# Performance work log

Hardware: AMD Instinct MI355X
Metric: run time of the kernel (lower is better)

The kernel has to match this reference:

```python
import jax, jax.numpy as jnp
import numpy as np
from jax import lax


def _conv(x, w, b):
    y = lax.conv_general_dilated(x, w, window_strides=(1, 1), padding='SAME',
                                 dimension_numbers=('NCHW', 'OIHW', 'NCHW'))
    return y + b[None, :, None, None]


def _maxpool2(x):
    return lax.reduce_window(x, -jnp.inf, lax.max,
                             window_dimensions=(1, 1, 2, 2),
                             window_strides=(1, 1, 2, 2), padding='VALID')


def setup_inputs() -> dict:
    key = jax.random.key(0)
    ks = jax.random.split(key, 11)
    f32 = jnp.float32
    return {
        'x': jax.random.normal(ks[0], (512, 1, 112, 112), f32),
        'w_conv1': jax.random.normal(ks[1], (8, 1, 3, 3), f32) * 0.1,
        'b_conv1': jax.random.normal(ks[2], (8,), f32) * 0.1,
        'w_conv2': jax.random.normal(ks[3], (16, 8, 3, 3), f32) * 0.1,
        'b_conv2': jax.random.normal(ks[4], (16,), f32) * 0.1,
        'w_patch': jax.random.normal(ks[5], (4, 64), f32) * 0.1,
        'b_patch': jax.random.normal(ks[6], (4,), f32) * 0.1,
        'w_fc1': jax.random.normal(ks[7], (64, 784), f32) * 0.05,
        'b_fc1': jax.random.normal(ks[8], (64,), f32) * 0.05,
        'w_fc2': jax.random.normal(ks[9], (10, 64), f32) * 0.05,
        'b_fc2': jax.random.normal(ks[10], (10,), f32) * 0.05,
    }


def reference(x, w_conv1, b_conv1, w_conv2, b_conv2, w_patch, b_patch,
              w_fc1, b_fc1, w_fc2, b_fc2):
    B = x.shape[0]
    h = _maxpool2(jax.nn.relu(_conv(x, w_conv1, b_conv1)))        # [B,8,56,56]
    f = _maxpool2(jax.nn.relu(_conv(h, w_conv2, b_conv2)))        # [B,16,28,28]
    C, H, W = f.shape[1], f.shape[2], f.shape[3]
    # im2col: 2x2 non-overlapping spatial patches, flattened as (C,2,2) -> 64
    p = f.reshape(B, C, H // 2, 2, W // 2, 2)
    p = p.transpose(0, 2, 4, 1, 3, 5).reshape(B, (H // 2) * (W // 2), C * 4)  # [B,196,64]
    pf = jnp.einsum('bpk,ok->bpo', p, w_patch) + b_patch          # [B,196,4]
    pf = pf.reshape(B, -1)                                        # [B,784]
    h1 = jax.nn.relu(pf @ w_fc1.T + b_fc1)
    logits = h1 @ w_fc2.T + b_fc2
    return jax.nn.log_softmax(logits, axis=-1)
```

## Files before the change

kernel.cpp:

```cpp
#include <hip/hip_runtime.h>


#define HSTR 58
#define NROWS 30
#define FSTR 33

typedef _Float16 half2_t __attribute__((ext_vector_type(2)));
typedef _Float16 f16x8 __attribute__((ext_vector_type(8)));
typedef float f32x4 __attribute__((ext_vector_type(4)));
typedef float f32x2 __attribute__((ext_vector_type(2)));

__device__ __forceinline__ unsigned pack_f16(float a, float b) {
  union { half2_t h; unsigned u; } z;
  z.h[0] = (_Float16)a;
  z.h[1] = (_Float16)b;
  return z.u;
}

__device__ __forceinline__ half2_t as_h2(unsigned u) {
  union { unsigned u; half2_t h; } z;
  z.u = u;
  return z.h;
}

__device__ __forceinline__ f16x8 as_f16x8(uint4 u) {
  union { uint4 u; f16x8 f; } z;
  z.u = u;
  return z.f;
}

__device__ __forceinline__ float fdot2_(half2_t a, half2_t b, float c) {
#if __has_builtin(__builtin_amdgcn_fdot2)
  return __builtin_amdgcn_fdot2(a, b, c, false);
#else
  return c + (float)a[0] * (float)b[0] + (float)a[1] * (float)b[1];
#endif
}

__global__ __launch_bounds__(256, 4) void k_fused(
    const float* __restrict__ x, const float* __restrict__ w1,
    const float* __restrict__ b1, const float* __restrict__ w2,
    const float* __restrict__ b2, const float* __restrict__ wp,
    const float* __restrict__ bp, const float* __restrict__ w_fc1,
    float* __restrict__ h1p) {
  __shared__ __align__(16) unsigned hsu[4 * NROWS * HSTR];
  __shared__ __align__(16) unsigned bwl[768];
  __shared__ __align__(16) unsigned wps[128];
  __shared__ __align__(16) unsigned fsu[49 * FSTR];
  __shared__ __align__(16) float pfl[392];
  const int tid = threadIdx.x;
  const int b = blockIdx.x >> 1;
  const int s = blockIdx.x & 1;
  const int l = tid & 63;
  const int wv = __builtin_amdgcn_readfirstlane(tid >> 6);
  const float* xb = x + (long)b * 12544;
  const float bpv = bp[tid & 3];

  for (int i = tid; i < 4 * NROWS * HSTR; i += 256) hsu[i] = 0u;
  for (int t = tid; t < 768; t += 256) {
    int oc = t / 48, k32 = t % 48;
    unsigned v = 0u;
    if (k32 < 36) {
      int icp = k32 / 9, tap = k32 - icp * 9;
      v = pack_f16(w2[(oc * 8 + 2 * icp) * 9 + tap],
                   w2[(oc * 8 + 2 * icp + 1) * 9 + tap]);
    }
    bwl[t] = v;
  }
  if (tid < 128) {
    int i = tid >> 2, ot = tid & 3;
    int l0 = 2 * i, l1 = 2 * i + 1;
    wps[tid] = pack_f16(wp[ot * 64 + (l0 & 15) * 4 + (l0 >> 4)],
                        wp[ot * 64 + (l1 & 15) * 4 + (l1 >> 4)]);
  }
  __syncthreads();

  for (int task = tid; task < 1680; task += 256) {
    int r = task / 56, hc = task % 56;
    int gr = 28 * s - 1 + r;
    if ((unsigned)gr >= 56u) continue;
    float win[4][4];
    int iy0 = 2 * gr - 1, ix0 = 2 * hc - 1;
#pragma unroll
    for (int rr = 0; rr < 4; ++rr) {
      int iy = iy0 + rr;
      bool yok = (unsigned)iy < 112u;
#pragma unroll
      for (int qq = 0; qq < 4; ++qq) {
        int ix = ix0 + qq;
        win[rr][qq] = (yok && (unsigned)ix < 112u) ? xb[iy * 112 + ix] : 0.f;
      }
    }
    float hv[8];
#pragma unroll
    for (int c = 0; c < 8; ++c) {
      f32x2 sA = {0.f, 0.f};
      f32x2 sB = {0.f, 0.f};
#pragma unroll
      for (int ty = 0; ty < 3; ++ty)
#pragma unroll
        for (int tx = 0; tx < 3; ++tx) {
          float wk = w1[c * 9 + ty * 3 + tx];
          f32x2 wkk = {wk, wk};
          f32x2 xa = {win[ty][tx], win[ty][tx + 1]};
          f32x2 xb2 = {win[ty + 1][tx], win[ty + 1][tx + 1]};
          sA = __builtin_elementwise_fma(xa, wkk, sA);
          sB = __builtin_elementwise_fma(xb2, wkk, sB);
        }
      f32x2 sm = __builtin_elementwise_max(sA, sB);
      float m = fmaxf(sm.x, sm.y);
      hv[c] = fmaxf(m + b1[c], 0.f);
    }
#pragma unroll
    for (int cp = 0; cp < 4; ++cp)
      hsu[(cp * NROWS + r) * HSTR + 1 + hc] = pack_f16(hv[2 * cp], hv[2 * cp + 1]);
  }
  __syncthreads();

  {
    const int q = l >> 4;
    int offs[12];
#pragma unroll
    for (int kk = 0; kk < 3; ++kk)
#pragma unroll
      for (int i = 0; i < 4; ++i) {
        int k32 = kk * 16 + q * 4 + i;
        int icp = k32 / 9, tap = k32 - icp * 9;
        int ty = tap / 3, tx = tap - ty * 3;
        offs[kk * 4 + i] = (icp * NROWS + ty) * HSTR + tx;
      }
    const int yoff = 2 * ((l >> 3) & 1) + ((l >> 1) & 1);
    const int xoff = 2 * ((l >> 2) & 1) + (l & 1);
    uint4 bu0 = *(const uint4*)(bwl + (l & 15) * 48 + 0 * 16 + q * 4);
    uint4 bu1 = *(const uint4*)(bwl + (l & 15) * 48 + 1 * 16 + q * 4);
    uint4 bu2 = *(const uint4*)(bwl + (l & 15) * 48 + 2 * 16 + q * 4);
    const float b2v = b2[l & 15];
    _Float16* fsh = (_Float16*)fsu;

#pragma unroll 1
    for (int c = 0; c < 2; ++c) {
#pragma unroll 2
      for (int p_l = wv; p_l < 49; p_l += 4) {
        int p = c * 49 + p_l;
        int py = p / 14, px = p - py * 14;
        int base = (4 * py + yoff) * HSTR + 4 * px + xoff;
        uint4 a0u, a1u, a2u = make_uint4(0u, 0u, 0u, 0u);
        a0u.x = hsu[base + offs[0]];
        a0u.y = hsu[base + offs[1]];
        a0u.z = hsu[base + offs[2]];
        a0u.w = hsu[base + offs[3]];
        a1u.x = hsu[base + offs[4]];
        a1u.y = hsu[base + offs[5]];
        a1u.z = hsu[base + offs[6]];
        a1u.w = hsu[base + offs[7]];
        if (q == 0) {
          a2u.x = hsu[base + offs[8]];
          a2u.y = hsu[base + offs[9]];
          a2u.z = hsu[base + offs[10]];
          a2u.w = hsu[base + offs[11]];
        }
        f32x4 acc = {0.f, 0.f, 0.f, 0.f};
        acc = __builtin_amdgcn_mfma_f32_16x16x32_f16(as_f16x8(a0u), as_f16x8(bu0), acc, 0, 0, 0);
        acc = __builtin_amdgcn_mfma_f32_16x16x32_f16(as_f16x8(a1u), as_f16x8(bu1), acc, 0, 0, 0);
        acc = __builtin_amdgcn_mfma_f32_16x16x32_f16(as_f16x8(a2u), as_f16x8(bu2), acc, 0, 0, 0);
        float mx = fmaxf(fmaxf(acc[0], acc[1]), fmaxf(acc[2], acc[3]));
        float fv = fmaxf(mx + b2v, 0.f);
        fsh[p_l * (2 * FSTR) + l] = (_Float16)fv;
      }
      __syncthreads();
      if (tid < 196) {
        int row = tid >> 2, ot = tid & 3;
        int p = c * 49 + row;
        const unsigned* fr = fsu + row * FSTR;
        float acc = 0.f;
#pragma unroll
        for (int i = 0; i < 32; ++i)
          acc = fdot2_(as_h2(fr[i]), as_h2(wps[i * 4 + ot]), acc);
        pfl[p * 4 + ot] = acc + bpv;
      }
      __syncthreads();
    }
  }

  {
    int j = tid >> 2, q4 = tid & 3;
    const float2* wrow = (const float2*)(w_fc1 + j * 784 + 392 * s + q4 * 98);
    const float2* pv = (const float2*)(pfl + q4 * 98);
    float acc = 0.f;
#pragma unroll 7
    for (int m = 0; m < 49; ++m) {
      float2 wv2 = wrow[m], fv2 = pv[m];
      acc += wv2.x * fv2.x + wv2.y * fv2.y;
    }
    acc += __shfl_down(acc, 2, 4);
    acc += __shfl_down(acc, 1, 4);
    if (q4 == 0) h1p[((long)b * 2 + s) * 64 + j] = acc;
  }
}

__global__ __launch_bounds__(64) void k_tail(const float* __restrict__ h1p,
                                             const float* __restrict__ b_fc1,
                                             const float* __restrict__ w_fc2,
                                             const float* __restrict__ b_fc2,
                                             float* __restrict__ out) {
  __shared__ float h1s[64];
  __shared__ float red[11];
  int b = blockIdx.x, j = threadIdx.x;
  float v = b_fc1[j] + h1p[(long)b * 128 + j] + h1p[(long)b * 128 + 64 + j];
  h1s[j] = fmaxf(v, 0.f);
  __syncthreads();
  if (j < 10) {
    float acc = b_fc2[j];
    const float* wo = w_fc2 + j * 64;
#pragma unroll
    for (int k = 0; k < 64; ++k) acc += h1s[k] * wo[k];
    red[j] = acc;
  }
  __syncthreads();
  if (j == 0) {
    float mx = red[0];
    for (int o = 1; o < 10; ++o) mx = fmaxf(mx, red[o]);
    float se = 0.f;
    for (int o = 0; o < 10; ++o) se += expf(red[o] - mx);
    red[10] = mx + logf(se);
  }
  __syncthreads();
  if (j < 10) out[b * 10 + j] = red[j] - red[10];
}

extern "C" void kernel_launch(void* const* d_in, const int* in_sizes, int n_in,
                              void* d_out, int out_size, void* d_ws, size_t ws_size,
                              hipStream_t stream) {
  const float* x = (const float*)d_in[0];
  const float* w1 = (const float*)d_in[1];
  const float* b1 = (const float*)d_in[2];
  const float* w2 = (const float*)d_in[3];
  const float* b2 = (const float*)d_in[4];
  const float* wp = (const float*)d_in[5];
  const float* bp = (const float*)d_in[6];
  const float* wf1 = (const float*)d_in[7];
  const float* bf1 = (const float*)d_in[8];
  const float* wf2 = (const float*)d_in[9];
  const float* bf2 = (const float*)d_in[10];

  float* h1p = (float*)d_ws;

  k_fused<<<dim3(1024), 256, 0, stream>>>(x, w1, b1, w2, b2, wp, bp, wf1, h1p);
  k_tail<<<dim3(512), 64, 0, stream>>>(h1p, bf1, wf2, bf2, (float*)d_out);
}
```

Before: 120.2 us.

## Split each image into four 2D quadrant tiles and rewrite tail as wave-per-sample

Measured after the change: 121.5 us. No clear change (+1.1%).

```diff
diff --git a/kernel.cpp b/kernel.cpp
--- a/kernel.cpp
+++ b/kernel.cpp
@@ -1,7 +1,7 @@
 #include <hip/hip_runtime.h>
 
 
-#define HSTR 58
+#define HSTR 36
 #define NROWS 30
 #define FSTR 33
 
@@ -37,7 +37,7 @@
 #endif
 }
 
-__global__ __launch_bounds__(256, 4) void k_fused(
+__global__ __launch_bounds__(256, 5) void k_fused(
     const float* __restrict__ x, const float* __restrict__ w1,
     const float* __restrict__ b1, const float* __restrict__ w2,
     const float* __restrict__ b2, const float* __restrict__ wp,
@@ -47,10 +47,12 @@
   __shared__ __align__(16) unsigned bwl[768];
   __shared__ __align__(16) unsigned wps[128];
   __shared__ __align__(16) unsigned fsu[49 * FSTR];
-  __shared__ __align__(16) float pfl[392];
+  __shared__ __align__(16) float pfl[196];
   const int tid = threadIdx.x;
-  const int b = blockIdx.x >> 1;
-  const int s = blockIdx.x & 1;
+  const int b = blockIdx.x >> 2;
+  const int tile = blockIdx.x & 3;
+  const int sr = tile >> 1;
+  const int sc = tile & 1;
   const int l = tid & 63;
   const int wv = __builtin_amdgcn_readfirstlane(tid >> 6);
   const float* xb = x + (long)b * 12544;
@@ -75,32 +77,42 @@
   }
   __syncthreads();
 
-  for (int task = tid; task < 1680; task += 256) {
-    int r = task / 56, hc = task % 56;
-    int gr = 28 * s - 1 + r;
-    if ((unsigned)gr >= 56u) continue;
+  for (int task = tid; task < 900; task += 256) {
+    int r = task / 30, c = task - r * 30;
+    int gr = 28 * sr - 1 + r;
+    int gc = 28 * sc - 1 + c;
+    if ((unsigned)gr >= 56u || (unsigned)gc >= 56u) continue;
     float win[4][4];
-    int iy0 = 2 * gr - 1, ix0 = 2 * hc - 1;
-#pragma unroll
-    for (int rr = 0; rr < 4; ++rr) {
-      int iy = iy0 + rr;
-      bool yok = (unsigned)iy < 112u;
-#pragma unroll
-      for (int qq = 0; qq < 4; ++qq) {
-        int ix = ix0 + qq;
-        win[rr][qq] = (yok && (unsigned)ix < 112u) ? xb[iy * 112 + ix] : 0.f;
+    int iy0 = 2 * gr - 1, ix0 = 2 * gc - 1;
+    if (gr >= 1 && gr <= 54 && gc >= 1 && gc <= 54) {
+      const float* xp = xb + iy0 * 112 + ix0;
+#pragma unroll
+      for (int rr = 0; rr < 4; ++rr)
+#pragma unroll
+        for (int qq = 0; qq < 4; ++qq)
+          win[rr][qq] = xp[rr * 112 + qq];
+    } else {
+#pragma unroll
+      for (int rr = 0; rr < 4; ++rr) {
+        int iy = iy0 + rr;
+        bool yok = (unsigned)iy < 112u;
+#pragma unroll
+        for (int qq = 0; qq < 4; ++qq) {
+          int ix = ix0 + qq;
+          win[rr][qq] = (yok && (unsigned)ix < 112u) ? xb[iy * 112 + ix] : 0.f;
+        }
       }
     }
     float hv[8];
 #pragma unroll
-    for (int c = 0; c < 8; ++c) {
+    for (int ch = 0; ch < 8; ++ch) {
       f32x2 sA = {0.f, 0.f};
       f32x2 sB = {0.f, 0.f};
 #pragma unroll
       for (int ty = 0; ty < 3; ++ty)
 #pragma unroll
         for (int tx = 0; tx < 3; ++tx) {
-          float wk = w1[c * 9 + ty * 3 + tx];
+          float wk = w1[ch * 9 + ty * 3 + tx];
           f32x2 wkk = {wk, wk};
           f32x2 xa = {win[ty][tx], win[ty][tx + 1]};
           f32x2 xb2 = {win[ty + 1][tx], win[ty + 1][tx + 1]};
@@ -109,11 +121,11 @@
         }
       f32x2 sm = __builtin_elementwise_max(sA, sB);
       float m = fmaxf(sm.x, sm.y);
-      hv[c] = fmaxf(m + b1[c], 0.f);
+      hv[ch] = fmaxf(m + b1[ch], 0.f);
     }
 #pragma unroll
     for (int cp = 0; cp < 4; ++cp)
-      hsu[(cp * NROWS + r) * HSTR + 1 + hc] = pack_f16(hv[2 * cp], hv[2 * cp + 1]);
+      hsu[(cp * NROWS + r) * HSTR + c] = pack_f16(hv[2 * cp], hv[2 * cp + 1]);
   }
   __syncthreads();
 
@@ -137,95 +149,93 @@
     const float b2v = b2[l & 15];
     _Float16* fsh = (_Float16*)fsu;
 
-#pragma unroll 1
-    for (int c = 0; c < 2; ++c) {
 #pragma unroll 2
-      for (int p_l = wv; p_l < 49; p_l += 4) {
-        int p = c * 49 + p_l;
-        int py = p / 14, px = p - py * 14;
-        int base = (4 * py + yoff) * HSTR + 4 * px + xoff;
-        uint4 a0u, a1u, a2u = make_uint4(0u, 0u, 0u, 0u);
-        a0u.x = hsu[base + offs[0]];
-        a0u.y = hsu[base + offs[1]];
-        a0u.z = hsu[base + offs[2]];
-        a0u.w = hsu[base + offs[3]];
-        a1u.x = hsu[base + offs[4]];
-        a1u.y = hsu[base + offs[5]];
-        a1u.z = hsu[base + offs[6]];
-        a1u.w = hsu[base + offs[7]];
-        if (q == 0) {
-          a2u.x = hsu[base + offs[8]];
-          a2u.y = hsu[base + offs[9]];
-          a2u.z = hsu[base + offs[10]];
-          a2u.w = hsu[base + offs[11]];
-        }
-        f32x4 acc = {0.f, 0.f, 0.f, 0.f};
-        acc = __builtin_amdgcn_mfma_f32_16x16x32_f16(as_f16x8(a0u), as_f16x8(bu0), acc, 0, 0, 0);
-        acc = __builtin_amdgcn_mfma_f32_16x16x32_f16(as_f16x8(a1u), as_f16x8(bu1), acc, 0, 0, 0);
-        acc = __builtin_amdgcn_mfma_f32_16x16x32_f16(as_f16x8(a2u), as_f16x8(bu2), acc, 0, 0, 0);
-        float mx = fmaxf(fmaxf(acc[0], acc[1]), fmaxf(acc[2], acc[3]));
-        float fv = fmaxf(mx + b2v, 0.f);
-        fsh[p_l * (2 * FSTR) + l] = (_Float16)fv;
+    for (int p_l = wv; p_l < 49; p_l += 4) {
+      int py = p_l / 7, px = p_l - py * 7;
+      int base = (4 * py + yoff) * HSTR + 4 * px + xoff;
+      uint4 a0u, a1u, a2u = make_uint4(0u, 0u, 0u, 0u);
+      a0u.x = hsu[base + offs[0]];
+      a0u.y = hsu[base + offs[1]];
+      a0u.z = hsu[base + offs[2]];
+      a0u.w = hsu[base + offs[3]];
+      a1u.x = hsu[base + offs[4]];
+      a1u.y = hsu[base + offs[5]];
+      a1u.z = hsu[base + offs[6]];
+      a1u.w = hsu[base + offs[7]];
+      if (q == 0) {
+        a2u.x = hsu[base + offs[8]];
+        a2u.y = hsu[base + offs[9]];
+        a2u.z = hsu[base + offs[10]];
+        a2u.w = hsu[base + offs[11]];
       }
-      __syncthreads();
-      if (tid < 196) {
-        int row = tid >> 2, ot = tid & 3;
-        int p = c * 49 + row;
-        const unsigned* fr = fsu + row * FSTR;
-        float acc = 0.f;
-#pragma unroll
-        for (int i = 0; i < 32; ++i)
-          acc = fdot2_(as_h2(fr[i]), as_h2(wps[i * 4 + ot]), acc);
-        pfl[p * 4 + ot] = acc + bpv;
-      }
-      __syncthreads();
-    }
+      f32x4 acc = {0.f, 0.f, 0.f, 0.f};
+      acc = __builtin_amdgcn_mfma_f32_16x16x32_f16(as_f16x8(a0u), as_f16x8(bu0), acc, 0, 0, 0);
+      acc = __builtin_amdgcn_mfma_f32_16x16x32_f16(as_f16x8(a1u), as_f16x8(bu1), acc, 0, 0, 0);
+      acc = __builtin_amdgcn_mfma_f32_16x16x32_f16(as_f16x8(a2u), as_f16x8(bu2), acc, 0, 0, 0);
+      float mx = fmaxf(fmaxf(acc[0], acc[1]), fmaxf(acc[2], acc[3]));
+      float fv = fmaxf(mx + b2v, 0.f);
+      fsh[p_l * (2 * FSTR) + l] = (_Float16)fv;
+    }
+    __syncthreads();
+    if (tid < 196) {
+      int row = tid >> 2, ot = tid & 3;
+      const unsigned* fr = fsu + row * FSTR;
+      float acc = 0.f;
+#pragma unroll
+      for (int i = 0; i < 32; ++i)
+        acc = fdot2_(as_h2(fr[i]), as_h2(wps[i * 4 + ot]), acc);
+      pfl[row * 4 + ot] = acc + bpv;
+    }
+    __syncthreads();
   }
 
   {
     int j = tid >> 2, q4 = tid & 3;
-    const float2* wrow = (const float2*)(w_fc1 + j * 784 + 392 * s + q4 * 98);
-    const float2* pv = (const float2*)(pfl + q4 * 98);
+    const float* wrow = w_fc1 + j * 784;
     float acc = 0.f;
-#pragma unroll 7
-    for (int m = 0; m < 49; ++m) {
-      float2 wv2 = wrow[m], fv2 = pv[m];
-      acc += wv2.x * fv2.x + wv2.y * fv2.y;
+#pragma unroll 4
+    for (int lp = q4; lp < 49; lp += 4) {
+      int Pl = lp / 7, Ql = lp - Pl * 7;
+      int gp = (7 * sr + Pl) * 14 + 7 * sc + Ql;
+      float4 w4 = *(const float4*)(wrow + gp * 4);
+      float4 p4 = *(const float4*)(pfl + lp * 4);
+      acc += w4.x * p4.x + w4.y * p4.y + w4.z * p4.z + w4.w * p4.w;
     }
     acc += __shfl_down(acc, 2, 4);
     acc += __shfl_down(acc, 1, 4);
-    if (q4 == 0) h1p[((long)b * 2 + s) * 64 + j] = acc;
-  }
-}
-
-__global__ __launch_bounds__(64) void k_tail(const float* __restrict__ h1p,
-                                             const float* __restrict__ b_fc1,
-                                             const float* __restrict__ w_fc2,
-                                             const float* __restrict__ b_fc2,
-                                             float* __restrict__ out) {
-  __shared__ float h1s[64];
-  __shared__ float red[11];
-  int b = blockIdx.x, j = threadIdx.x;
-  float v = b_fc1[j] + h1p[(long)b * 128 + j] + h1p[(long)b * 128 + 64 + j];
-  h1s[j] = fmaxf(v, 0.f);
-  __syncthreads();
-  if (j < 10) {
-    float acc = b_fc2[j];
-    const float* wo = w_fc2 + j * 64;
-#pragma unroll
-    for (int k = 0; k < 64; ++k) acc += h1s[k] * wo[k];
-    red[j] = acc;
-  }
-  __syncthreads();
-  if (j == 0) {
-    float mx = red[0];
-    for (int o = 1; o < 10; ++o) mx = fmaxf(mx, red[o]);
-    float se = 0.f;
-    for (int o = 0; o < 10; ++o) se += expf(red[o] - mx);
-    red[10] = mx + logf(se);
-  }
-  __syncthreads();
-  if (j < 10) out[b * 10 + j] = red[j] - red[10];
+    if (q4 == 0) h1p[((long)b * 4 + tile) * 64 + j] = acc;
+  }
+}
+
+__global__ __launch_bounds__(256) void k_tail(const float* __restrict__ h1p,
+                                              const float* __restrict__ b_fc1,
+                                              const float* __restrict__ w_fc2,
+                                              const float* __restrict__ b_fc2,
+                                              float* __restrict__ out) {
+  const int l = threadIdx.x & 63;
+  const int wv = threadIdx.x >> 6;
+  const int b = blockIdx.x * 4 + wv;
+  const float* hp = h1p + (long)b * 256;
+  float v = b_fc1[l] + hp[l] + hp[64 + l] + hp[128 + l] + hp[192 + l];
+  float h = fmaxf(v, 0.f);
+  float lg[10];
+#pragma unroll
+  for (int o = 0; o < 10; ++o) {
+    float t = h * w_fc2[o * 64 + l];
+#pragma unroll
+    for (int off = 32; off; off >>= 1) t += __shfl_xor(t, off);
+    lg[o] = t + b_fc2[o];
+  }
+  float mx = lg[0];
+#pragma unroll
+  for (int o = 1; o < 10; ++o) mx = fmaxf(mx, lg[o]);
+  float se = 0.f;
+#pragma unroll
+  for (int o = 0; o < 10; ++o) se += __expf(lg[o] - mx);
+  float ls = mx + __logf(se);
+#pragma unroll
+  for (int o = 0; o < 10; ++o)
+    if (l == o) out[b * 10 + o] = lg[o] - ls;
 }
 
 extern "C" void kernel_launch(void* const* d_in, const int* in_sizes, int n_in,
@@ -245,6 +255,6 @@
 
   float* h1p = (float*)d_ws;
 
-  k_fused<<<dim3(1024), 256, 0, stream>>>(x, w1, b1, w2, b2, wp, bp, wf1, h1p);
-  k_tail<<<dim3(512), 64, 0, stream>>>(h1p, bf1, wf2, bf2, (float*)d_out);
-}
+  k_fused<<<dim3(2048), 256, 0, stream>>>(x, w1, b1, w2, b2, wp, bp, wf1, h1p);
+  k_tail<<<dim3(128), 256, 0, stream>>>(h1p, bf1, wf2, bf2, (float*)d_out);
+}
```
